# Kernel tuning notes

Measured on AMD Instinct MI355X. Metric: run time of the kernel, lower is better.

The kernel has to match this reference:

```python
import jax, jax.numpy as jnp
import numpy as np

B, A = 4096, 8          # episodes, agents per episode
N = B * A               # total nodes
E = B * A * (A - 1)     # fully-connected directed edges within each group
F_IN, D, H, M, NA = 64, 64, 4, 64, 10  # in_feat, gnn_dim, heads, mem_dim, n_actions
NEG_SLOPE = 0.2
LN_EPS = 1e-5


def _build_edge_index():
    base = np.arange(A)
    s = np.repeat(base, A)
    d = np.tile(base, A)
    keep = s != d
    s, d = s[keep], d[keep]                       # [A*(A-1)]
    offs = (np.arange(B) * A)[:, None]
    src = (offs + s[None, :]).reshape(-1)
    dst = (offs + d[None, :]).reshape(-1)
    return jnp.asarray(np.stack([src, dst]), dtype=jnp.int32)  # [2, E]


def setup_inputs() -> dict:
    key = jax.random.key(0)
    ks = jax.random.split(key, 16)
    sc = 0.05
    return {
        "x": jax.random.normal(ks[0], (N, F_IN), jnp.float32),
        "edge_attr": jax.random.normal(ks[1], (E, 3), jnp.float32),
        "hidden": jax.random.normal(ks[2], (N, M), jnp.float32) * sc,
        "edge_index": _build_edge_index(),
        # GATv2 params
        "Wl": jax.random.normal(ks[3], (H * D, F_IN), jnp.float32) * sc,
        "bl": jnp.zeros((H * D,), jnp.float32),
        "Wr": jax.random.normal(ks[4], (H * D, F_IN), jnp.float32) * sc,
        "br": jnp.zeros((H * D,), jnp.float32),
        "We": jax.random.normal(ks[5], (H * D, 3), jnp.float32) * sc,
        "be": jnp.zeros((H * D,), jnp.float32),
        "att": jax.random.normal(ks[6], (H, D), jnp.float32) * sc,
        "bias_g": jnp.zeros((D,), jnp.float32),
        # GRUCell params (gate order r,z,n as in torch)
        "W_ih": jax.random.normal(ks[7], (3 * M, D), jnp.float32) * sc,
        "W_hh": jax.random.normal(ks[8], (3 * M, M), jnp.float32) * sc,
        "b_ih": jnp.zeros((3 * M,), jnp.float32),
        "b_hh": jnp.zeros((3 * M,), jnp.float32),
        # LayerNorm + output Linear
        "ln_g": jnp.ones((M,), jnp.float32),
        "ln_b": jnp.zeros((M,), jnp.float32),
        "Wq": jax.random.normal(ks[9], (NA, M), jnp.float32) * sc,
        "bq": jnp.zeros((NA,), jnp.float32),
    }


def reference(x, edge_attr, hidden, edge_index, Wl, bl, Wr, br, We, be, att,
              bias_g, W_ih, W_hh, b_ih, b_hh, ln_g, ln_b, Wq, bq):
    src, dst = edge_index[0], edge_index[1]
    # GATv2Conv (concat=False -> mean over heads), share_weights=False
    xl = (x @ Wl.T + bl).reshape(N, H, D)          # source projection
    xr = (x @ Wr.T + br).reshape(N, H, D)          # target projection
    ee = (edge_attr @ We.T + be).reshape(E, H, D)  # edge embedding
    m = jax.nn.leaky_relu(xl[src] + xr[dst] + ee, NEG_SLOPE)  # [E,H,D]
    logits = jnp.einsum('ehd,hd->eh', m, att)                  # [E,H]
    lmax = jax.ops.segment_max(logits, dst, num_segments=N)    # [N,H]
    ex = jnp.exp(logits - lmax[dst])
    denom = jax.ops.segment_sum(ex, dst, num_segments=N)       # [N,H]
    alpha = ex / denom[dst]                                    # softmax per target
    agg = jax.ops.segment_sum(alpha[:, :, None] * xl[src], dst, num_segments=N)  # [N,H,D]
    h_gnn = jax.nn.relu(agg.mean(axis=1) + bias_g)             # [N,D]
    # GRUCell
    gi = h_gnn @ W_ih.T + b_ih
    gh = hidden @ W_hh.T + b_hh
    ir, iz, inn = jnp.split(gi, 3, axis=-1)
    hr, hz, hn = jnp.split(gh, 3, axis=-1)
    r = jax.nn.sigmoid(ir + hr)
    z = jax.nn.sigmoid(iz + hz)
    n = jnp.tanh(inn + r * hn)
    h = (1.0 - z) * n + z * hidden                              # [N,M]
    # LayerNorm + Linear head
    mu = h.mean(axis=-1, keepdims=True)
    var = ((h - mu) ** 2).mean(axis=-1, keepdims=True)
    hln = (h - mu) / jnp.sqrt(var + LN_EPS) * ln_g + ln_b
    q = hln @ Wq.T + bq                                         # [N,NA]
    return q, h
```

## Files before the change

### kernel.cpp

```cpp
#include <hip/hip_runtime.h>

typedef unsigned short u16;
typedef __attribute__((ext_vector_type(8))) short bf16x8;
typedef __attribute__((ext_vector_type(4))) float f32x4;
typedef _Float16 f16;
typedef __attribute__((ext_vector_type(2))) f16 h2;
typedef __attribute__((ext_vector_type(8))) f16 h8;

#define NAG 8
#define NAGB 16
#define FIN 64
#define MDIM 64
#define NACT 10
#define EPG 56
#define NTOT 32768
#define ABP 72
#define XLS 296
#define XHS 72

#define U_XR  4736
#define U_RZ  0
#define U_HN  2048
#define U_LN  3072
#define U_HG  6144
#define U_INB 8320

__device__ __forceinline__ float b2f(u16 u) {
  return __uint_as_float(((unsigned int)u) << 16);
}
__device__ __forceinline__ u16 f2b(float f) {
  unsigned int x = __float_as_uint(f);
  unsigned int r = x + 0x7fffu + ((x >> 16) & 1u);
  return (u16)(r >> 16);
}
__device__ __forceinline__ u16 f2h(float f) {
  f16 h = (f16)f; u16 u; __builtin_memcpy(&u, &h, 2); return u;
}
__device__ __forceinline__ float h2f(u16 u) {
  f16 h; __builtin_memcpy(&h, &u, 2); return (float)h;
}

union H8u { h8 v; h2 p[4]; };

__device__ __forceinline__ h8 lrelu8(h8 m) {
  h8 s = m * (f16)0.2f;
#if __has_builtin(__builtin_elementwise_max)
  return __builtin_elementwise_max(m, s);
#else
  h8 r;
#pragma unroll
  for (int i = 0; i < 8; i++) r[i] = (m[i] > s[i]) ? m[i] : s[i];
  return r;
#endif
}

__device__ __forceinline__ float dotacc(h2 a, h2 b, float c) {
  c += (float)a[0] * (float)b[0];
  c += (float)a[1] * (float)b[1];
  return c;
}

__global__ __launch_bounds__(256) void prep_weights(
    const float* __restrict__ Wl, const float* __restrict__ Wr,
    const float* __restrict__ Wih, const float* __restrict__ Whh,
    u16* __restrict__ wsB)
{
  const int idx = blockIdx.x * 256 + threadIdx.x;
  if (idx >= 56 * 2 * 64) return;
  const int L  = idx & 63;
  const int ks = (idx >> 6) & 1;
  const int T  = idx >> 7;
  const float* W; int row0;
  if      (T < 16) { W = Wl;  row0 = T * 16; }
  else if (T < 32) { W = Wr;  row0 = (T - 16) * 16; }
  else if (T < 44) { W = Wih; row0 = (T - 32) * 16; }
  else             { W = Whh; row0 = (T - 44) * 16; }
  const int row = row0 + (L & 15);
  const int k0  = ks * 32 + (L >> 4) * 8;
  u16 v[8];
#pragma unroll
  for (int j = 0; j < 8; j++) v[j] = f2b(W[row * 64 + k0 + j]);
  *(bf16x8*)(wsB + (size_t)idx * 8) = *(bf16x8*)v;
}

__global__ __launch_bounds__(256, 6) void gnn_rnn_kernel(
    const float* __restrict__ x, const float* __restrict__ edge_attr,
    const float* __restrict__ hidden,
    const float* __restrict__ bl, const float* __restrict__ br,
    const float* __restrict__ We, const float* __restrict__ be,
    const float* __restrict__ att, const float* __restrict__ bias_g,
    const float* __restrict__ b_ih, const float* __restrict__ b_hh,
    const float* __restrict__ ln_g, const float* __restrict__ ln_b,
    const float* __restrict__ Wq, const float* __restrict__ bq,
    const u16* __restrict__ wsB,
    float* __restrict__ d_out)
{
  __shared__ __align__(16) char uraw[18944];
  __shared__ __align__(16) u16 u2raw[NAGB * ABP];
  __shared__ __align__(16) u16 s_hidb[NAGB * ABP];
  __shared__ __align__(16) u16 s_w0h[256], s_w1h[256], s_w2h[256], s_atth[256];

  u16*   uXL  = (u16*)uraw;
  u16*   uXR  = (u16*)uraw + U_XR;
  u16*   uInn = (u16*)uraw + U_INB;
  u16*   s_hgb = (u16*)uraw + U_HG;
  float* uF   = (float*)uraw;
  u16*   s_xb = u2raw;
  float (*s_alpha)[4] = (float(*)[4])u2raw;

  const int t = threadIdx.x;
  const int b = blockIdx.x;
  const int L = t & 63;
  const int w = t >> 6;
  const int q = L >> 4;

  {
    const float* xb = x + b * (NAGB * FIN);
    const float* hb = hidden + b * (NAGB * MDIM);
#pragma unroll
    for (int i = t; i < NAGB * FIN; i += 256) {
      const int a = i >> 6, m = i & 63;
      s_xb[a * ABP + m] = f2b(xb[i]);
      s_hidb[a * ABP + m] = f2b(hb[i]);
    }
    s_w0h[t]  = f2h(We[t * 3]);
    s_w1h[t]  = f2h(We[t * 3 + 1]);
    s_w2h[t]  = f2h(We[t * 3 + 2]);
    s_atth[t] = f2h(att[t]);
  }
  float ea00 = 0.f, ea01 = 0.f, ea02 = 0.f, ea10 = 0.f, ea11 = 0.f, ea12 = 0.f;
  if (L < EPG) {
    const float* eb = edge_attr + b * (2 * EPG * 3) + L * 3;
    ea00 = eb[0]; ea01 = eb[1]; ea02 = eb[2];
    ea10 = eb[EPG * 3]; ea11 = eb[EPG * 3 + 1]; ea12 = eb[EPG * 3 + 2];
  }
  __syncthreads();

  {
    const int arow = L & 15;
    bf16x8 af0 = *(const bf16x8*)&s_xb[arow * ABP + q * 8];
    bf16x8 af1 = *(const bf16x8*)&s_xb[arow * ABP + 32 + q * 8];
    const bf16x8* wsBv = (const bf16x8*)wsB;
#pragma unroll 4
    for (int i = 0; i < 8; i++) {
      const int T = w * 8 + i;
      f32x4 acc = {0.f, 0.f, 0.f, 0.f};
      acc = __builtin_amdgcn_mfma_f32_16x16x32_bf16(af0, wsBv[(T * 2 + 0) * 64 + L], acc, 0, 0, 0);
      acc = __builtin_amdgcn_mfma_f32_16x16x32_bf16(af1, wsBv[(T * 2 + 1) * 64 + L], acc, 0, 0, 0);
      const int col = L & 15;
      const int Tm = T & 15;
      const int h = Tm >> 2, d = (Tm & 3) * 16 + col;
      const int gc = Tm * 16 + col;
      if (T < 16) {
        const float bias = bl[gc];
#pragma unroll
        for (int r = 0; r < 4; r++)
          uXL[(q * 4 + r) * XLS + h * XHS + d] = f2h(acc[r] + bias);
      } else {
        const float bias = br[gc] + be[gc];
#pragma unroll
        for (int r = 0; r < 4; r++)
          uXR[(q * 4 + r) * XLS + h * XHS + d] = f2h(acc[r] + bias);
      }
    }
  }
  __syncthreads();

  {
    const int h = w;
    if (L < EPG) {
      const int e = L;
      const int s = e / 7, k = e % 7;
      const int j = k + (k >= s ? 1 : 0);
      const f16 a00 = (f16)ea00, a01 = (f16)ea01, a02 = (f16)ea02;
      const f16 a10 = (f16)ea10, a11 = (f16)ea11, a12 = (f16)ea12;
      const u16* xlp0 = uXL + s * XLS + h * XHS;
      const u16* xrp0 = uXR + j * XLS + h * XHS;
      const u16* xlp1 = uXL + (8 + s) * XLS + h * XHS;
      const u16* xrp1 = uXR + (8 + j) * XLS + h * XHS;
      const u16* w0p = s_w0h + h * 64;
      const u16* w1p = s_w1h + h * 64;
      const u16* w2p = s_w2h + h * 64;
      const u16* atp = s_atth + h * 64;
      float lgA0 = 0.f, lgB0 = 0.f, lgA1 = 0.f, lgB1 = 0.f;
#pragma unroll 2
      for (int kq = 0; kq < 8; kq++) {
        H8u w0, w1, w2, at, x0, r0, x1, r1, m0, m1;
        w0.v = *(const h8*)(w0p + kq * 8);
        w1.v = *(const h8*)(w1p + kq * 8);
        w2.v = *(const h8*)(w2p + kq * 8);
        at.v = *(const h8*)(atp + kq * 8);
        x0.v = *(const h8*)(xlp0 + kq * 8);
        r0.v = *(const h8*)(xrp0 + kq * 8);
        x1.v = *(const h8*)(xlp1 + kq * 8);
        r1.v = *(const h8*)(xrp1 + kq * 8);
        m0.v = x0.v + r0.v + w0.v * a00 + w1.v * a01 + w2.v * a02;
        m0.v = lrelu8(m0.v);
        m1.v = x1.v + r1.v + w0.v * a10 + w1.v * a11 + w2.v * a12;
        m1.v = lrelu8(m1.v);
        lgA0 = dotacc(m0.p[0], at.p[0], lgA0);
        lgB0 = dotacc(m0.p[1], at.p[1], lgB0);
        lgA0 = dotacc(m0.p[2], at.p[2], lgA0);
        lgB0 = dotacc(m0.p[3], at.p[3], lgB0);
        lgA1 = dotacc(m1.p[0], at.p[0], lgA1);
        lgB1 = dotacc(m1.p[1], at.p[1], lgB1);
        lgA1 = dotacc(m1.p[2], at.p[2], lgA1);
        lgB1 = dotacc(m1.p[3], at.p[3], lgB1);
      }
      s_alpha[e][h]       = lgA0 + lgB0;
      s_alpha[EPG + e][h] = lgA1 + lgB1;
    }
  }
  __syncthreads();

  if (L < 16) {
    const int ep = w & 1;
    const int j = ((w >> 1) << 2) + (L >> 2);
    const int h = L & 3;
    const int e0 = ep * EPG;
    float mx = -1e30f;
#pragma unroll
    for (int s = 0; s < 8; s++) {
      if (s == j) continue;
      int e = e0 + s * 7 + (j > s ? j - 1 : j);
      mx = fmaxf(mx, s_alpha[e][h]);
    }
    float sum = 0.f;
#pragma unroll
    for (int s = 0; s < 8; s++) {
      if (s == j) continue;
      int e = e0 + s * 7 + (j > s ? j - 1 : j);
      float ex = __expf(s_alpha[e][h] - mx);
      s_alpha[e][h] = ex;
      sum += ex;
    }
    float inv = 1.f / sum;
#pragma unroll
    for (int s = 0; s < 8; s++) {
      if (s == j) continue;
      int e = e0 + s * 7 + (j > s ? j - 1 : j);
      s_alpha[e][h] *= inv;
    }
  }
  __syncthreads();

  {
    const int ep = t >> 7, jj = (t >> 4) & 7, dq = t & 15;
    const int a16 = ep * 8 + jj;
    float acc[4] = {0.f, 0.f, 0.f, 0.f};
#pragma unroll 2
    for (int h = 0; h < 4; h++) {
#pragma unroll
      for (int s = 0; s < 8; s++) {
        if (s == jj) continue;
        int e = ep * EPG + s * 7 + (jj > s ? jj - 1 : jj);
        float al = s_alpha[e][h];
        const u16* xp = uXL + (ep * 8 + s) * XLS + h * XHS + dq * 4;
        ushort4 xv = *(const ushort4*)xp;
        acc[0] += al * h2f(xv.x);
        acc[1] += al * h2f(xv.y);
        acc[2] += al * h2f(xv.z);
        acc[3] += al * h2f(xv.w);
      }
    }
    const f32x4 bg = *(const f32x4*)(bias_g + dq * 4);
    u16 pk[4];
#pragma unroll
    for (int c = 0; c < 4; c++) {
      float v = acc[c] * 0.25f + bg[c];
      pk[c] = f2b(v > 0.f ? v : 0.f);
    }
    *(uint2*)&s_hgb[a16 * ABP + dq * 4] = *(uint2*)pk;
  }
  __syncthreads();

  {
    const int arow = L & 15;
    bf16x8 ag0 = *(const bf16x8*)&s_hgb[arow * ABP + q * 8];
    bf16x8 ag1 = *(const bf16x8*)&s_hgb[arow * ABP + 32 + q * 8];
    bf16x8 ah0 = *(const bf16x8*)&s_hidb[arow * ABP + q * 8];
    bf16x8 ah1 = *(const bf16x8*)&s_hidb[arow * ABP + 32 + q * 8];
    const bf16x8* wsBv = (const bf16x8*)wsB;
#pragma unroll
    for (int i = 0; i < 3; i++) {
      const int T6 = w * 3 + i;
      const int Tg = 32 + T6, Th = 44 + T6;
      f32x4 acci = {0.f, 0.f, 0.f, 0.f};
      acci = __builtin_amdgcn_mfma_f32_16x16x32_bf16(ag0, wsBv[(Tg * 2 + 0) * 64 + L], acci, 0, 0, 0);
      acci = __builtin_amdgcn_mfma_f32_16x16x32_bf16(ag1, wsBv[(Tg * 2 + 1) * 64 + L], acci, 0, 0, 0);
      f32x4 acch = {0.f, 0.f, 0.f, 0.f};
      acch = __builtin_amdgcn_mfma_f32_16x16x32_bf16(ah0, wsBv[(Th * 2 + 0) * 64 + L], acch, 0, 0, 0);
      acch = __builtin_amdgcn_mfma_f32_16x16x32_bf16(ah1, wsBv[(Th * 2 + 1) * 64 + L], acch, 0, 0, 0);
      const int col = L & 15;
      const int gc = T6 * 16 + col;
      if (T6 < 8) {
        const float bsum = b_ih[gc] + b_hh[gc];
#pragma unroll
        for (int r = 0; r < 4; r++)
          uF[U_RZ + (q * 4 + r) * 128 + gc] = acci[r] + acch[r] + bsum;
      } else {
        const float bi = b_ih[gc], bh = b_hh[gc];
#pragma unroll
        for (int r = 0; r < 4; r++) {
          uInn[(q * 4 + r) * 64 + gc - 128] = f2b(acci[r] + bi);
          uF[U_HN + (q * 4 + r) * 64 + gc - 128] = acch[r] + bh;
        }
      }
    }
  }
  __syncthreads();

  {
    const float lng = ln_g[L];
    const float lnb = ln_b[L];
#pragma unroll
    for (int rr = 0; rr < 4; rr++) {
      const int a = w + rr * 4, m = L;
      float rz_r = uF[U_RZ + a * 128 + m];
      float rz_z = uF[U_RZ + a * 128 + 64 + m];
      float inn  = b2f(uInn[a * 64 + m]);
      float hn   = uF[U_HN + a * 64 + m];
      float hid  = b2f(s_hidb[a * ABP + m]);
      float r = 1.f / (1.f + __expf(-rz_r));
      float z = 1.f / (1.f + __expf(-rz_z));
      float xg = inn + r * hn;
      xg = fminf(fmaxf(xg, -20.f), 20.f);
      float e2 = __expf(2.f * xg);
      float n = (e2 - 1.f) / (e2 + 1.f);
      float hv = (1.f - z) * n + z * hid;
      d_out[NTOT * NACT + (b * NAGB + a) * MDIM + m] = hv;
      float sum = hv, sq = hv * hv;
#pragma unroll
      for (int off = 1; off < 64; off <<= 1) {
        sum += __shfl_xor(sum, off, 64);
        sq  += __shfl_xor(sq,  off, 64);
      }
      float mu  = sum * (1.f / 64.f);
      float var = sq * (1.f / 64.f) - mu * mu;
      var = var > 0.f ? var : 0.f;
      uF[U_LN + a * 68 + m] = (hv - mu) * rsqrtf(var + 1e-5f) * lng + lnb;
    }
  }
  __syncthreads();

  if (t < NAGB * NACT) {
    const int a = t / NACT, o = t % NACT;
    float acc = bq[o];
    const float4* lv = (const float4*)(uF + U_LN + a * 68);
    const float4* wv = (const float4*)(Wq + o * 64);
#pragma unroll 4
    for (int kq = 0; kq < 16; kq++) {
      float4 l4 = lv[kq], w4 = wv[kq];
      acc += l4.x * w4.x + l4.y * w4.y + l4.z * w4.z + l4.w * w4.w;
    }
    d_out[(b * NAGB + a) * NACT + o] = acc;
  }
}

extern "C" void kernel_launch(void* const* d_in, const int* in_sizes, int n_in,
                              void* d_out, int out_size, void* d_ws, size_t ws_size,
                              hipStream_t stream) {
  const int N  = in_sizes[0] / FIN;
  const int Bn = N / NAGB;
  u16* wsB = (u16*)d_ws;

  prep_weights<<<28, 256, 0, stream>>>(
      (const float*)d_in[4],
      (const float*)d_in[6],
      (const float*)d_in[12],
      (const float*)d_in[13],
      wsB);

  gnn_rnn_kernel<<<Bn, 256, 0, stream>>>(
      (const float*)d_in[0], (const float*)d_in[1], (const float*)d_in[2],
      (const float*)d_in[5],
      (const float*)d_in[7],
      (const float*)d_in[8],
      (const float*)d_in[9],
      (const float*)d_in[10],
      (const float*)d_in[11],
      (const float*)d_in[14],
      (const float*)d_in[15],
      (const float*)d_in[16], (const float*)d_in[17],
      (const float*)d_in[18], (const float*)d_in[19],
      wsB, (float*)d_out);
}
```

Baseline: 145.3 us.

## Load x/hidden into registers, fuse softmax into aggregation, use fdot2

Measured after the change: 144.6 us. No clear change (-0.5%).

```diff
diff --git a/kernel.cpp b/kernel.cpp
--- a/kernel.cpp
+++ b/kernel.cpp
@@ -39,6 +39,12 @@
 __device__ __forceinline__ float h2f(u16 u) {
   f16 h; __builtin_memcpy(&h, &u, 2); return (float)h;
 }
+__device__ __forceinline__ bf16x8 pack8(f32x4 a, f32x4 b) {
+  u16 v[8];
+#pragma unroll
+  for (int c = 0; c < 4; c++) { v[c] = f2b(a[c]); v[c + 4] = f2b(b[c]); }
+  return *(bf16x8*)v;
+}
 
 union H8u { h8 v; h2 p[4]; };
 
@@ -54,11 +60,17 @@
 #endif
 }
 
+#if __has_builtin(__builtin_amdgcn_fdot2)
+__device__ __forceinline__ float dotacc(h2 a, h2 b, float c) {
+  return __builtin_amdgcn_fdot2(a, b, c, false);
+}
+#else
 __device__ __forceinline__ float dotacc(h2 a, h2 b, float c) {
   c += (float)a[0] * (float)b[0];
   c += (float)a[1] * (float)b[1];
   return c;
 }
+#endif
 
 __global__ __launch_bounds__(256) void prep_weights(
     const float* __restrict__ Wl, const float* __restrict__ Wr,
@@ -83,7 +95,7 @@
   *(bf16x8*)(wsB + (size_t)idx * 8) = *(bf16x8*)v;
 }
 
-__global__ __launch_bounds__(256, 6) void gnn_rnn_kernel(
+__global__ __launch_bounds__(256, 7) void gnn_rnn_kernel(
     const float* __restrict__ x, const float* __restrict__ edge_attr,
     const float* __restrict__ hidden,
     const float* __restrict__ bl, const float* __restrict__ br,
@@ -96,8 +108,7 @@
     float* __restrict__ d_out)
 {
   __shared__ __align__(16) char uraw[18944];
-  __shared__ __align__(16) u16 u2raw[NAGB * ABP];
-  __shared__ __align__(16) u16 s_hidb[NAGB * ABP];
+  __shared__ __align__(16) u16 s_alpha[2 * 8 * 4 * 8];
   __shared__ __align__(16) u16 s_w0h[256], s_w1h[256], s_w2h[256], s_atth[256];
 
   u16*   uXL  = (u16*)uraw;
@@ -105,41 +116,35 @@
   u16*   uInn = (u16*)uraw + U_INB;
   u16*   s_hgb = (u16*)uraw + U_HG;
   float* uF   = (float*)uraw;
-  u16*   s_xb = u2raw;
-  float (*s_alpha)[4] = (float(*)[4])u2raw;
 
   const int t = threadIdx.x;
   const int b = blockIdx.x;
   const int L = t & 63;
   const int w = t >> 6;
   const int q = L >> 4;
-
-  {
-    const float* xb = x + b * (NAGB * FIN);
-    const float* hb = hidden + b * (NAGB * MDIM);
-#pragma unroll
-    for (int i = t; i < NAGB * FIN; i += 256) {
-      const int a = i >> 6, m = i & 63;
-      s_xb[a * ABP + m] = f2b(xb[i]);
-      s_hidb[a * ABP + m] = f2b(hb[i]);
-    }
-    s_w0h[t]  = f2h(We[t * 3]);
-    s_w1h[t]  = f2h(We[t * 3 + 1]);
-    s_w2h[t]  = f2h(We[t * 3 + 2]);
-    s_atth[t] = f2h(att[t]);
-  }
+  const int arow = L & 15;
+
+  const float* xb = x + b * (NAGB * FIN);
+  const float* hb = hidden + b * (NAGB * MDIM);
+  f32x4 xa0 = *(const f32x4*)(xb + arow * 64 + q * 8);
+  f32x4 xa1 = *(const f32x4*)(xb + arow * 64 + q * 8 + 4);
+  f32x4 xa2 = *(const f32x4*)(xb + arow * 64 + 32 + q * 8);
+  f32x4 xa3 = *(const f32x4*)(xb + arow * 64 + 32 + q * 8 + 4);
+
+  s_w0h[t]  = f2h(We[t * 3]);
+  s_w1h[t]  = f2h(We[t * 3 + 1]);
+  s_w2h[t]  = f2h(We[t * 3 + 2]);
+  s_atth[t] = f2h(att[t]);
   float ea00 = 0.f, ea01 = 0.f, ea02 = 0.f, ea10 = 0.f, ea11 = 0.f, ea12 = 0.f;
   if (L < EPG) {
     const float* eb = edge_attr + b * (2 * EPG * 3) + L * 3;
     ea00 = eb[0]; ea01 = eb[1]; ea02 = eb[2];
     ea10 = eb[EPG * 3]; ea11 = eb[EPG * 3 + 1]; ea12 = eb[EPG * 3 + 2];
   }
-  __syncthreads();
-
-  {
-    const int arow = L & 15;
-    bf16x8 af0 = *(const bf16x8*)&s_xb[arow * ABP + q * 8];
-    bf16x8 af1 = *(const bf16x8*)&s_xb[arow * ABP + 32 + q * 8];
+
+  {
+    bf16x8 af0 = pack8(xa0, xa1);
+    bf16x8 af1 = pack8(xa2, xa3);
     const bf16x8* wsBv = (const bf16x8*)wsB;
 #pragma unroll 4
     for (int i = 0; i < 8; i++) {
@@ -207,61 +212,44 @@
         lgA1 = dotacc(m1.p[2], at.p[2], lgA1);
         lgB1 = dotacc(m1.p[3], at.p[3], lgB1);
       }
-      s_alpha[e][h]       = lgA0 + lgB0;
-      s_alpha[EPG + e][h] = lgA1 + lgB1;
-    }
-  }
-  __syncthreads();
-
-  if (L < 16) {
-    const int ep = w & 1;
-    const int j = ((w >> 1) << 2) + (L >> 2);
-    const int h = L & 3;
-    const int e0 = ep * EPG;
-    float mx = -1e30f;
-#pragma unroll
-    for (int s = 0; s < 8; s++) {
-      if (s == j) continue;
-      int e = e0 + s * 7 + (j > s ? j - 1 : j);
-      mx = fmaxf(mx, s_alpha[e][h]);
-    }
-    float sum = 0.f;
-#pragma unroll
-    for (int s = 0; s < 8; s++) {
-      if (s == j) continue;
-      int e = e0 + s * 7 + (j > s ? j - 1 : j);
-      float ex = __expf(s_alpha[e][h] - mx);
-      s_alpha[e][h] = ex;
-      sum += ex;
-    }
-    float inv = 1.f / sum;
-#pragma unroll
-    for (int s = 0; s < 8; s++) {
-      if (s == j) continue;
-      int e = e0 + s * 7 + (j > s ? j - 1 : j);
-      s_alpha[e][h] *= inv;
-    }
-  }
-  __syncthreads();
-
+      s_alpha[((    j) * 4 + h) * 8 + s] = f2h(__expf(lgA0 + lgB0));
+      s_alpha[((8 + j) * 4 + h) * 8 + s] = f2h(__expf(lgA1 + lgB1));
+    } else {
+      const int j2 = L - EPG;
+      s_alpha[((    j2) * 4 + w) * 8 + j2] = 0;
+      s_alpha[((8 + j2) * 4 + w) * 8 + j2] = 0;
+    }
+  }
+  __syncthreads();
+
+  f32x4 ha0 = *(const f32x4*)(hb + arow * 64 + q * 8);
+  f32x4 ha1 = *(const f32x4*)(hb + arow * 64 + q * 8 + 4);
+  f32x4 ha2 = *(const f32x4*)(hb + arow * 64 + 32 + q * 8);
+  f32x4 ha3 = *(const f32x4*)(hb + arow * 64 + 32 + q * 8 + 4);
   {
     const int ep = t >> 7, jj = (t >> 4) & 7, dq = t & 15;
     const int a16 = ep * 8 + jj;
     float acc[4] = {0.f, 0.f, 0.f, 0.f};
-#pragma unroll 2
+#pragma unroll
     for (int h = 0; h < 4; h++) {
+      H8u av;
+      av.v = *(const h8*)&s_alpha[(a16 * 4 + h) * 8];
+      float den = 0.f;
+      float ah[4] = {0.f, 0.f, 0.f, 0.f};
 #pragma unroll
       for (int s = 0; s < 8; s++) {
-        if (s == jj) continue;
-        int e = ep * EPG + s * 7 + (jj > s ? jj - 1 : jj);
-        float al = s_alpha[e][h];
+        float al = (float)av.v[s];
+        den += al;
         const u16* xp = uXL + (ep * 8 + s) * XLS + h * XHS + dq * 4;
         ushort4 xv = *(const ushort4*)xp;
-        acc[0] += al * h2f(xv.x);
-        acc[1] += al * h2f(xv.y);
-        acc[2] += al * h2f(xv.z);
-        acc[3] += al * h2f(xv.w);
-      }
+        ah[0] += al * h2f(xv.x);
+        ah[1] += al * h2f(xv.y);
+        ah[2] += al * h2f(xv.z);
+        ah[3] += al * h2f(xv.w);
+      }
+      const float inv = 1.f / den;
+#pragma unroll
+      for (int c = 0; c < 4; c++) acc[c] += ah[c] * inv;
     }
     const f32x4 bg = *(const f32x4*)(bias_g + dq * 4);
     u16 pk[4];
@@ -272,14 +260,16 @@
     }
     *(uint2*)&s_hgb[a16 * ABP + dq * 4] = *(uint2*)pk;
   }
-  __syncthreads();
-
-  {
-    const int arow = L & 15;
+  bf16x8 ah0 = pack8(ha0, ha1);
+  bf16x8 ah1 = pack8(ha2, ha3);
+  __syncthreads();
+
+  float hidr[4];
+#pragma unroll
+  for (int rr = 0; rr < 4; rr++) hidr[rr] = hb[(w + rr * 4) * 64 + L];
+  {
     bf16x8 ag0 = *(const bf16x8*)&s_hgb[arow * ABP + q * 8];
     bf16x8 ag1 = *(const bf16x8*)&s_hgb[arow * ABP + 32 + q * 8];
-    bf16x8 ah0 = *(const bf16x8*)&s_hidb[arow * ABP + q * 8];
-    bf16x8 ah1 = *(const bf16x8*)&s_hidb[arow * ABP + 32 + q * 8];
     const bf16x8* wsBv = (const bf16x8*)wsB;
 #pragma unroll
     for (int i = 0; i < 3; i++) {
@@ -320,7 +310,7 @@
       float rz_z = uF[U_RZ + a * 128 + 64 + m];
       float inn  = b2f(uInn[a * 64 + m]);
       float hn   = uF[U_HN + a * 64 + m];
-      float hid  = b2f(s_hidb[a * ABP + m]);
+      float hid  = hidr[rr];
       float r = 1.f / (1.f + __expf(-rz_r));
       float z = 1.f / (1.f + __expf(-rz_z));
       float xg = inn + r * hn;
```
